# Performance work log

Hardware: AMD Instinct MI355X
Metric: run time of the kernel (lower is better)

Reference implementation:

```python
import jax, jax.numpy as jnp
import numpy as np

N_HEAD = 12
HEAD_DIM = 64
N_EMBD = 768
ATTN_MULT = 0.125
B, T = 2, 2048
NEG_INF = -1e30


def setup_inputs() -> dict:
    key = jax.random.key(0)
    ks = jax.random.split(key, 3)
    x = jax.random.normal(ks[0], (B, T, N_EMBD), dtype=jnp.float32)
    W_attn = jax.random.normal(ks[1], (N_EMBD, 3 * N_HEAD * HEAD_DIM), dtype=jnp.float32) * 0.02
    b_attn = jnp.zeros((3 * N_HEAD * HEAD_DIM,), dtype=jnp.float32)
    W_proj = jax.random.normal(ks[2], (N_HEAD * HEAD_DIM, N_EMBD), dtype=jnp.float32) * 0.02
    b_proj = jnp.zeros((N_EMBD,), dtype=jnp.float32)
    return {"x": x, "W_attn": W_attn, "b_attn": b_attn, "W_proj": W_proj, "b_proj": b_proj}


def reference(x, W_attn, b_attn, W_proj, b_proj):
    Bsz, Tlen, C = x.shape
    H, D = N_HEAD, HEAD_DIM
    qkv = x @ W_attn + b_attn                       # [B,T,3*H*D]
    q, k, v = jnp.split(qkv, 3, axis=-1)
    q = q.reshape(Bsz, Tlen, H, D).transpose(0, 2, 1, 3)   # [B,H,T,D]
    k = k.reshape(Bsz, Tlen, H, D).transpose(0, 2, 1, 3)
    v = v.reshape(Bsz, Tlen, H, D).transpose(0, 2, 1, 3)

    att = jnp.einsum('bhtd,bhsd->bhts', q, k) * ATTN_MULT  # [B,H,T,T]
    causal = jnp.tril(jnp.ones((Tlen, Tlen), dtype=bool))  # [T,T]
    att = jnp.where(causal, att, NEG_INF)

    # selection mask from head 0 (SelectionHeadLinearComboKind.NONE)
    S = jax.nn.relu(att[:, 0:1, :, :])                     # [B,1,T,T]; relu kills -inf
    # protect_bos_token: zero column 0 (key index 0)
    col = jnp.arange(Tlen)
    S = S * (col[None, None, None, :] != 0)
    # prevent_from_masking_myself: zero diagonal
    S = S * (1.0 - jnp.eye(Tlen, dtype=S.dtype))

    # accumulate selection over query (row) axis: ProtectionKind.NONE
    FF = jnp.cumsum(S, axis=-2)                            # [B,1,T,T]
    att = att - FF                                         # broadcast over heads

    p = jax.nn.softmax(att, axis=-1)                       # [B,H,T,T]
    y = jnp.einsum('bhts,bhsd->bhtd', p, v)                # [B,H,T,D]
    y = y.transpose(0, 2, 1, 3).reshape(Bsz, Tlen, H * D)  # [B,T,H*D]
    return y @ W_proj + b_proj
```

## Files before the change

kernel.cpp:

```cpp
#include <hip/hip_runtime.h>
#include <math.h>

#define T 2048
#define NH 12
#define HD 64
#define C3 2304
#define CE 768
#define NB 2

typedef __attribute__((ext_vector_type(8))) short bf16x8;
typedef __attribute__((ext_vector_type(4))) float f32x4;
typedef __attribute__((ext_vector_type(16))) float f32x16;
typedef __attribute__((ext_vector_type(4))) unsigned u32x4;

__device__ inline void bf16split(float a, unsigned short& h, unsigned short& l) {
    unsigned int u = __float_as_uint(a);
    unsigned int r = (u + 0x7FFFu + ((u >> 16) & 1u)) >> 16;
    h = (unsigned short)r;
    float hf = __uint_as_float(r << 16);
    float lo = a - hf;
    unsigned int v = __float_as_uint(lo);
    l = (unsigned short)((v + 0x7FFFu + ((v >> 16) & 1u)) >> 16);
}

// ... 7 lines not shown
__global__ __launch_bounds__(256) void cvt_split_kernel(const float* __restrict__ A,
        unsigned short* __restrict__ H, unsigned short* __restrict__ L) {
    int i = blockIdx.x * 256 + threadIdx.x;
    float4 a0 = *(reinterpret_cast<const float4*>(A) + (size_t)i * 2);
    float4 a1 = *(reinterpret_cast<const float4*>(A) + (size_t)i * 2 + 1);
    float f[8] = {a0.x, a0.y, a0.z, a0.w, a1.x, a1.y, a1.z, a1.w};
    unsigned short h[8], l[8];
    #pragma unroll
    for (int j = 0; j < 8; ++j) bf16split(f[j], h[j], l[j]);
    uint4 hv, lv;
    hv.x = (unsigned)h[0] | ((unsigned)h[1] << 16); hv.y = (unsigned)h[2] | ((unsigned)h[3] << 16);
    hv.z = (unsigned)h[4] | ((unsigned)h[5] << 16); hv.w = (unsigned)h[6] | ((unsigned)h[7] << 16);
    lv.x = (unsigned)l[0] | ((unsigned)l[1] << 16); lv.y = (unsigned)l[2] | ((unsigned)l[3] << 16);
    lv.z = (unsigned)l[4] | ((unsigned)l[5] << 16); lv.w = (unsigned)l[6] | ((unsigned)l[7] << 16);
    reinterpret_cast<uint4*>(H)[i] = hv;
    reinterpret_cast<uint4*>(L)[i] = lv;
}

__global__ __launch_bounds__(256) void cvt_split_T_kernel(const float* __restrict__ W,
        unsigned short* __restrict__ H, unsigned short* __restrict__ L, int K, int N) {
    __shared__ float tile[64][65];
    const int n0 = blockIdx.x * 64, k0 = blockIdx.y * 64;
    const int t = threadIdx.x;
    {
        int r = t >> 2, c4 = (t & 3) * 16;
        #pragma unroll
        for (int u = 0; u < 4; ++u) {
            float4 w = *reinterpret_cast<const float4*>(&W[(size_t)(k0 + r) * N + n0 + c4 + u * 4]);
            tile[r][c4 + u * 4 + 0] = w.x; tile[r][c4 + u * 4 + 1] = w.y;
            tile[r][c4 + u * 4 + 2] = w.z; tile[r][c4 + u * 4 + 3] = w.w;
        }
    }
    __syncthreads();
    {
        int n = t >> 2, kc = (t & 3) * 16;
        unsigned short h[16], l[16];
        #pragma unroll
        for (int j = 0; j < 16; ++j) bf16split(tile[kc + j][n], h[j], l[j]);
        uint4 hv0, hv1, lv0, lv1;
        hv0.x = (unsigned)h[0] | ((unsigned)h[1] << 16);  hv0.y = (unsigned)h[2] | ((unsigned)h[3] << 16);
        hv0.z = (unsigned)h[4] | ((unsigned)h[5] << 16);  hv0.w = (unsigned)h[6] | ((unsigned)h[7] << 16);
        hv1.x = (unsigned)h[8] | ((unsigned)h[9] << 16);  hv1.y = (unsigned)h[10] | ((unsigned)h[11] << 16);
        hv1.z = (unsigned)h[12] | ((unsigned)h[13] << 16); hv1.w = (unsigned)h[14] | ((unsigned)h[15] << 16);
        lv0.x = (unsigned)l[0] | ((unsigned)l[1] << 16);  lv0.y = (unsigned)l[2] | ((unsigned)l[3] << 16);
        lv0.z = (unsigned)l[4] | ((unsigned)l[5] << 16);  lv0.w = (unsigned)l[6] | ((unsigned)l[7] << 16);
        lv1.x = (unsigned)l[8] | ((unsigned)l[9] << 16);  lv1.y = (unsigned)l[10] | ((unsigned)l[11] << 16);
        lv1.z = (unsigned)l[12] | ((unsigned)l[13] << 16); lv1.w = (unsigned)l[14] | ((unsigned)l[15] << 16);
        size_t o = (size_t)(n0 + n) * K + k0 + kc;
        reinterpret_cast<uint4*>(&H[o])[0] = hv0; reinterpret_cast<uint4*>(&H[o])[1] = hv1;
        reinterpret_cast<uint4*>(&L[o])[0] = lv0; reinterpret_cast<uint4*>(&L[o])[1] = lv1;
    }
}

__global__ __launch_bounds__(256) void cvt_qk_kernel(const float* __restrict__ qkv,
        unsigned short* __restrict__ Qh, unsigned short* __restrict__ Ql,
        unsigned short* __restrict__ Kh, unsigned short* __restrict__ Kl) {
    int t = blockIdx.x * 256 + threadIdx.x;
    int dg = t & 7;
    int s = (t >> 3) & (T - 1);
    int bh = t >> 14;
    int b = bh / NH, h = bh % NH;
    const float* qs = qkv + (size_t)(b * T + s) * C3 + h * 64 + dg * 8;
    const float* ks = qs + 768;
    size_t o = ((size_t)bh * T + s) * 64 + dg * 8;
    #pragma unroll
    for (int which = 0; which < 2; ++which) {
        const float* src = (which == 0) ? qs : ks;
        float4 a0 = *reinterpret_cast<const float4*>(src);
        float4 a1 = *reinterpret_cast<const float4*>(src + 4);
        float f[8] = {a0.x, a0.y, a0.z, a0.w, a1.x, a1.y, a1.z, a1.w};
        unsigned short hh[8], ll[8];
        #pragma unroll
        for (int j = 0; j < 8; ++j) bf16split(f[j], hh[j], ll[j]);
        uint4 hv, lv;
        hv.x = (unsigned)hh[0] | ((unsigned)hh[1] << 16); hv.y = (unsigned)hh[2] | ((unsigned)hh[3] << 16);
        hv.z = (unsigned)hh[4] | ((unsigned)hh[5] << 16); hv.w = (unsigned)hh[6] | ((unsigned)hh[7] << 16);
        lv.x = (unsigned)ll[0] | ((unsigned)ll[1] << 16); lv.y = (unsigned)ll[2] | ((unsigned)ll[3] << 16);
        lv.z = (unsigned)ll[4] | ((unsigned)ll[5] << 16); lv.w = (unsigned)ll[6] | ((unsigned)ll[7] << 16);
        if (which == 0) {
            *reinterpret_cast<uint4*>(&Qh[o]) = hv;
            *reinterpret_cast<uint4*>(&Ql[o]) = lv;
        } else {
            *reinterpret_cast<uint4*>(&Kh[o]) = hv;
            *reinterpret_cast<uint4*>(&Kl[o]) = lv;
        }
    }
}

__global__ __launch_bounds__(256) void cvt_kv_vt_kernel(const float* __restrict__ qkv,
        unsigned short* __restrict__ Vh, unsigned short* __restrict__ Vl) {
    __shared__ float tile[64][65];
    const int s0 = blockIdx.x * 64;
    const int bh = blockIdx.y;
    const int b = bh / NH, h = bh % NH;
    const int tid = threadIdx.x;
    {
        int r = tid >> 2, c0 = (tid & 3) * 16;
        const float* src = qkv + (size_t)(b * T + s0 + r) * C3 + 1536 + h * 64 + c0;
        #pragma unroll
        for (int u = 0; u < 4; ++u) {
            float4 w = *reinterpret_cast<const float4*>(src + u * 4);
            tile[r][c0 + u * 4 + 0] = w.x; tile[r][c0 + u * 4 + 1] = w.y;
            tile[r][c0 + u * 4 + 2] = w.z; tile[r][c0 + u * 4 + 3] = w.w;
        }
    }
    __syncthreads();
    {
        int d = tid >> 2, cs = (tid & 3) * 16;
        unsigned short hh[16], ll[16];
        #pragma unroll
        for (int j = 0; j < 16; ++j) bf16split(tile[cs + j][d], hh[j], ll[j]);
        uint4 hv0, hv1, lv0, lv1;
        hv0.x = (unsigned)hh[0] | ((unsigned)hh[1] << 16);  hv0.y = (unsigned)hh[2] | ((unsigned)hh[3] << 16);
        hv0.z = (unsigned)hh[4] | ((unsigned)hh[5] << 16);  hv0.w = (unsigned)hh[6] | ((unsigned)hh[7] << 16);
        hv1.x = (unsigned)hh[8] | ((unsigned)hh[9] << 16);  hv1.y = (unsigned)hh[10] | ((unsigned)hh[11] << 16);
        hv1.z = (unsigned)hh[12] | ((unsigned)hh[13] << 16); hv1.w = (unsigned)hh[14] | ((unsigned)hh[15] << 16);
        lv0.x = (unsigned)ll[0] | ((unsigned)ll[1] << 16);  lv0.y = (unsigned)ll[2] | ((unsigned)ll[3] << 16);
        lv0.z = (unsigned)ll[4] | ((unsigned)ll[5] << 16);  lv0.w = (unsigned)ll[6] | ((unsigned)ll[7] << 16);
        lv1.x = (unsigned)ll[8] | ((unsigned)ll[9] << 16);  lv1.y = (unsigned)ll[10] | ((unsigned)ll[11] << 16);
        lv1.z = (unsigned)ll[12] | ((unsigned)ll[13] << 16); lv1.w = (unsigned)ll[14] | ((unsigned)ll[15] << 16);
        size_t o = ((size_t)bh * 64 + d) * T + s0 + cs;
        reinterpret_cast<uint4*>(&Vh[o])[0] = hv0; reinterpret_cast<uint4*>(&Vh[o])[1] = hv1;
        reinterpret_cast<uint4*>(&Vl[o])[0] = lv0; reinterpret_cast<uint4*>(&Vl[o])[1] = lv1;
    }
}

#define LDST 40
__global__ __launch_bounds__(256) void gemm_mfma_kernel(
        const unsigned short* __restrict__ Ah, const unsigned short* __restrict__ Al,
        const unsigned short* __restrict__ Bh, const unsigned short* __restrict__ Bl,
        const float* __restrict__ bias, float* __restrict__ Cm,
        int M, int N, int K) {
    __shared__ unsigned short lA[2][128 * LDST];
    __shared__ unsigned short lB[2][128 * LDST];
    const int tid = threadIdx.x;
    const int bm = blockIdx.y * 128, bn = blockIdx.x * 128;
    const int lane = tid & 63, wid = tid >> 6;
    const int wr = wid >> 1, wc = wid & 1;
    f32x4 acc[4][4];
    #pragma unroll
    for (int i = 0; i < 4; ++i)
        #pragma unroll
        for (int j = 0; j < 4; ++j) acc[i][j] = (f32x4){0.f, 0.f, 0.f, 0.f};
    const int srow = tid >> 2, sk8 = (tid & 3) * 8;
    const int arb = wr * 64 + (lane & 15);
    const int brb = wc * 64 + (lane & 15);
    const int koff = (lane >> 4) * 8;
    for (int k0 = 0; k0 < K; k0 += 32) {
        __syncthreads();
        #pragma unroll
        for (int c = 0; c < 2; ++c) {
            int row = srow + 64 * c;
            uint4 va = *reinterpret_cast<const uint4*>(&Ah[(size_t)(bm + row) * K + k0 + sk8]);
            uint4 vb = *reinterpret_cast<const uint4*>(&Al[(size_t)(bm + row) * K + k0 + sk8]);
            uint4 vc = *reinterpret_cast<const uint4*>(&Bh[(size_t)(bn + row) * K + k0 + sk8]);
            uint4 vd = *reinterpret_cast<const uint4*>(&Bl[(size_t)(bn + row) * K + k0 + sk8]);
            *reinterpret_cast<uint4*>(&lA[0][row * LDST + sk8]) = va;
            *reinterpret_cast<uint4*>(&lA[1][row * LDST + sk8]) = vb;
            *reinterpret_cast<uint4*>(&lB[0][row * LDST + sk8]) = vc;
            *reinterpret_cast<uint4*>(&lB[1][row * LDST + sk8]) = vd;
        }
        __syncthreads();
        bf16x8 fa[2][4], fb[2][4];
        #pragma unroll
        for (int fi = 0; fi < 4; ++fi) {
            fa[0][fi] = *reinterpret_cast<const bf16x8*>(&lA[0][(arb + fi * 16) * LDST + koff]);
            fa[1][fi] = *reinterpret_cast<const bf16x8*>(&lA[1][(arb + fi * 16) * LDST + koff]);
            fb[0][fi] = *reinterpret_cast<const bf16x8*>(&lB[0][(brb + fi * 16) * LDST + koff]);
            fb[1][fi] = *reinterpret_cast<const bf16x8*>(&lB[1][(brb + fi * 16) * LDST + koff]);
        }
        #pragma unroll
        for (int fi = 0; fi < 4; ++fi)
            #pragma unroll
            for (int fj = 0; fj < 4; ++fj) {
                acc[fi][fj] = __builtin_amdgcn_mfma_f32_16x16x32_bf16(fa[0][fi], fb[0][fj], acc[fi][fj], 0, 0, 0);
                acc[fi][fj] = __builtin_amdgcn_mfma_f32_16x16x32_bf16(fa[0][fi], fb[1][fj], acc[fi][fj], 0, 0, 0);
                acc[fi][fj] = __builtin_amdgcn_mfma_f32_16x16x32_bf16(fa[1][fi], fb[0][fj], acc[fi][fj], 0, 0, 0);
            }
    }
    #pragma unroll
    for (int fj = 0; fj < 4; ++fj) {
        int col = bn + wc * 64 + fj * 16 + (lane & 15);
        float bv = bias[col];
        #pragma unroll
        for (int fi = 0; fi < 4; ++fi) {
            int row0 = bm + wr * 64 + fi * 16 + (lane >> 4) * 4;
            #pragma unroll
            for (int p = 0; p < 4; ++p)
                Cm[(size_t)(row0 + p) * N + col] = acc[fi][fj][p] + bv;
        }
    }
}

__global__ __launch_bounds__(256) void gemm_bias_kernel(
        const float* __restrict__ A, const float* __restrict__ B,
        const float* __restrict__ bias, float* __restrict__ Cm,
        int M, int N, int K) {
    __shared__ float As[16][64];
    __shared__ float Bs[16][68];
    const int tid = threadIdx.x;
    const int ty = tid >> 4, tx = tid & 15;
    const int bm = blockIdx.y * 64, bn = blockIdx.x * 64;
    float acc[4][4] = {};
    for (int k0 = 0; k0 < K; k0 += 16) {
        {
            int r = tid >> 2;
            int kk = (tid & 3) * 4;
            float4 a = *reinterpret_cast<const float4*>(&A[(size_t)(bm + r) * K + k0 + kk]);
            As[kk + 0][r] = a.x; As[kk + 1][r] = a.y; As[kk + 2][r] = a.z; As[kk + 3][r] = a.w;
        }
        {
            int kk = tid >> 4;
            int c = (tid & 15) * 4;
            *reinterpret_cast<float4*>(&Bs[kk][c]) =
                *reinterpret_cast<const float4*>(&B[(size_t)(k0 + kk) * N + bn + c]);
        }
        __syncthreads();
        #pragma unroll
        for (int kk = 0; kk < 16; ++kk) {
            float4 a4 = *reinterpret_cast<const float4*>(&As[kk][ty * 4]);
            float4 b4 = *reinterpret_cast<const float4*>(&Bs[kk][tx * 4]);
            float av[4] = {a4.x, a4.y, a4.z, a4.w};
            float bv[4] = {b4.x, b4.y, b4.z, b4.w};
            #pragma unroll
            for (int i = 0; i < 4; ++i)
                #pragma unroll
                for (int j = 0; j < 4; ++j)
                    acc[i][j] = fmaf(av[i], bv[j], acc[i][j]);
        }
        __syncthreads();
    }
    #pragma unroll
    for (int i = 0; i < 4; ++i) {
        int row = bm + ty * 4 + i;
        #pragma unroll
        for (int j = 0; j < 4; ++j) {
            int col = bn + tx * 4 + j;
            Cm[(size_t)row * N + col] = acc[i][j] + bias[col];
        }
    }
}

#define FST 72

__global__ __launch_bounds__(256) void s0_mfma_kernel(
        const unsigned short* __restrict__ Qh, const unsigned short* __restrict__ Ql,
        const unsigned short* __restrict__ Kh, const unsigned short* __restrict__ Kl,
        float* __restrict__ S) {
    const int kb = blockIdx.x * 64, qb = blockIdx.y * 64, b = blockIdx.z;
    const int tid = threadIdx.x;
    float* Sb = S + (size_t)b * T * T;
    if (kb > qb) {
        const int ty = tid >> 4, tx = tid & 15;
        #pragma unroll
        for (int i = 0; i < 4; ++i) {
            float4 z = {0.f, 0.f, 0.f, 0.f};
            *reinterpret_cast<float4*>(&Sb[(size_t)(qb + ty * 4 + i) * T + kb + tx * 4]) = z;
        }
        return;
    }
    const int lane = tid & 63, w = tid >> 6;
    const int fr = lane & 15, fg = lane >> 4;
    __shared__ unsigned short Ks[2][64 * FST];
    const int hb0 = b * NH;
    {
        const int sr = tid >> 2, sc0 = (tid & 3) * 16;
        const unsigned short* kh = Kh + ((size_t)hb0 * T + kb + sr) * 64 + sc0;
        const unsigned short* kl = Kl + ((size_t)hb0 * T + kb + sr) * 64 + sc0;
        uint4 a0 = reinterpret_cast<const uint4*>(kh)[0];
        uint4 a1 = reinterpret_cast<const uint4*>(kh)[1];
        uint4 b0 = reinterpret_cast<const uint4*>(kl)[0];
        uint4 b1 = reinterpret_cast<const uint4*>(kl)[1];
        *reinterpret_cast<uint4*>(&Ks[0][sr * FST + sc0 + 0]) = a0;
        *reinterpret_cast<uint4*>(&Ks[0][sr * FST + sc0 + 8]) = a1;
        *reinterpret_cast<uint4*>(&Ks[1][sr * FST + sc0 + 0]) = b0;
        *reinterpret_cast<uint4*>(&Ks[1][sr * FST + sc0 + 8]) = b1;
    }
    bf16x8 qh[2], ql[2];
    #pragma unroll
    for (int ks = 0; ks < 2; ++ks) {
        size_t qo = ((size_t)hb0 * T + qb + w * 16 + fr) * 64 + ks * 32 + fg * 8;
        qh[ks] = *reinterpret_cast<const bf16x8*>(&Qh[qo]);
        ql[ks] = *reinterpret_cast<const bf16x8*>(&Ql[qo]);
    }
    __syncthreads();
    f32x4 qk[4];
    #pragma unroll
    for (int fj = 0; fj < 4; ++fj) qk[fj] = (f32x4){0.f, 0.f, 0.f, 0.f};
    #pragma unroll
    for (int ks = 0; ks < 2; ++ks) {
        bf16x8 kbh[4], kbl[4];
        #pragma unroll
        for (int fj = 0; fj < 4; ++fj) {
            kbh[fj] = *reinterpret_cast<const bf16x8*>(&Ks[0][(fj * 16 + fr) * FST + ks * 32 + fg * 8]);
            kbl[fj] = *reinterpret_cast<const bf16x8*>(&Ks[1][(fj * 16 + fr) * FST + ks * 32 + fg * 8]);
        }
        #pragma unroll
        for (int fj = 0; fj < 4; ++fj) {
            qk[fj] = __builtin_amdgcn_mfma_f32_16x16x32_bf16(qh[ks], kbh[fj], qk[fj], 0, 0, 0);
            qk[fj] = __builtin_amdgcn_mfma_f32_16x16x32_bf16(qh[ks], kbl[fj], qk[fj], 0, 0, 0);
            qk[fj] = __builtin_amdgcn_mfma_f32_16x16x32_bf16(ql[ks], kbh[fj], qk[fj], 0, 0, 0);
        }
    }
    #pragma unroll
    for (int p = 0; p < 4; ++p) {
        int t = qb + w * 16 + fg * 4 + p;
        #pragma unroll
        for (int fj = 0; fj < 4; ++fj) {
            int s = kb + fj * 16 + fr;
            float v = qk[fj][p] * 0.125f;
            Sb[(size_t)t * T + s] = (s >= 1 && s < t) ? fmaxf(v, 0.0f) : 0.0f;
        }
    }
}

__global__ __launch_bounds__(256) void s0_kernel(const float* __restrict__ qkv,
                                                 float* __restrict__ S) {
    const int kb = blockIdx.x * 64, qb = blockIdx.y * 64, b = blockIdx.z;
    const int tid = threadIdx.x, ty = tid >> 4, tx = tid & 15;
    float* Sb = S + (size_t)b * T * T;
    if (kb > qb) {
        #pragma unroll
        for (int i = 0; i < 4; ++i) {
            int row = qb + ty * 4 + i;
            float4 z = {0.f, 0.f, 0.f, 0.f};
            *reinterpret_cast<float4*>(&Sb[(size_t)row * T + kb + tx * 4]) = z;
        }
        return;
    }
    __shared__ float Qt[64][68];
    __shared__ float Kt[64][68];
    {
        int r = tid >> 2;
        int c0 = (tid & 3) * 16;
        const float* qrow = qkv + (size_t)(b * T + qb + r) * C3 + 0;
        const float* krow = qkv + (size_t)(b * T + kb + r) * C3 + 768;
        #pragma unroll
        for (int u = 0; u < 4; ++u) {
            float4 q4 = *reinterpret_cast<const float4*>(&qrow[c0 + u * 4]);
            float4 k4 = *reinterpret_cast<const float4*>(&krow[c0 + u * 4]);
            int d = c0 + u * 4;
            Qt[d + 0][r] = q4.x; Qt[d + 1][r] = q4.y; Qt[d + 2][r] = q4.z; Qt[d + 3][r] = q4.w;
            Kt[d + 0][r] = k4.x; Kt[d + 1][r] = k4.y; Kt[d + 2][r] = k4.z; Kt[d + 3][r] = k4.w;
        }
    }
    __syncthreads();
    float acc[4][4] = {};
    #pragma unroll
    for (int d = 0; d < 64; ++d) {
        float4 qv = *reinterpret_cast<const float4*>(&Qt[d][ty * 4]);
        float4 kv = *reinterpret_cast<const float4*>(&Kt[d][tx * 4]);
        float qa[4] = {qv.x, qv.y, qv.z, qv.w};
        float ka[4] = {kv.x, kv.y, kv.z, kv.w};
        #pragma unroll
        for (int i = 0; i < 4; ++i)
            #pragma unroll
            for (int j = 0; j < 4; ++j)
                acc[i][j] = fmaf(qa[i], ka[j], acc[i][j]);
    }
    #pragma unroll
    for (int i = 0; i < 4; ++i) {
        int t = qb + ty * 4 + i;
        float o[4];
        #pragma unroll
        for (int j = 0; j < 4; ++j) {
            int s = kb + tx * 4 + j;
            float v = acc[i][j] * 0.125f;
            o[j] = (s >= 1 && s < t) ? fmaxf(v, 0.0f) : 0.0f;
        }
        float4 o4 = {o[0], o[1], o[2], o[3]};
        *reinterpret_cast<float4*>(&Sb[(size_t)t * T + kb + tx * 4]) = o4;
    }
}

__global__ __launch_bounds__(256) void colsum_kernel(const float* __restrict__ S,
                                                     float* __restrict__ Psum) {
    int s = blockIdx.x * 256 + threadIdx.x;
    int j = blockIdx.y, b = blockIdx.z;
    const float* Sb = S + (size_t)b * T * T;
    float sum = 0.f;
    for (int r = 0; r < 64; ++r) sum += Sb[(size_t)(j * 64 + r) * T + s];
    Psum[((size_t)b * 32 + j) * T + s] = sum;
}

__global__ __launch_bounds__(256) void scanseg_kernel(float* __restrict__ Psum) {
    int s = blockIdx.x * 256 + threadIdx.x;
    int b = blockIdx.y;
    float run = 0.f;
    for (int j = 0; j < 32; ++j) {
        size_t idx = ((size_t)b * 32 + j) * T + s;
        float v = Psum[idx];
        Psum[idx] = run;
        run += v;
    }
}

__global__ __launch_bounds__(256) void ffscan_kernel(float* __restrict__ S,
                                                     const float* __restrict__ Psum) {
    int s = blockIdx.x * 256 + threadIdx.x;
    int j = blockIdx.y, b = blockIdx.z;
    float run = Psum[((size_t)b * 32 + j) * T + s];
    float* Sb = S + (size_t)b * T * T;
    for (int r = 0; r < 64; ++r) {
        size_t idx = (size_t)(j * 64 + r) * T + s;
        run += Sb[idx];
        Sb[idx] = run;
    }
}

__device__ const int FTQ[40] = {15,15,15,15,14,14,14,13,13,13,12,12,12,11,11,11,10,10,9,9,8,8,7,7,6,5,4,3,14,10,6,2,13,9,5,1,12,8,4,0};
__device__ const int FK0[40] = {0,8,16,24,0,8,16,0,8,16,0,8,16,0,8,16,0,8,0,8,0,8,0,8,0,0,0,0,24,16,8,0,24,16,8,0,24,16,8,0};
__device__ const int FK1[40] = {8,16,24,32,8,16,24,8,16,24,8,16,24,8,16,24,8,16,8,16,8,16,8,16,8,8,8,8,30,22,14,6,28,20,12,4,26,18,10,2};
__device__ const int FCB[12] = {0,2,4,6,8,11,14,17,20,24,28,32};

__global__ __launch_bounds__(256) void flash_mfma_kernel(
        const unsigned short* __restrict__ Qh, const unsigned short* __restrict__ Ql,
        const unsigned short* __restrict__ Kh, const unsigned short* __restrict__ Kl,
        const unsigned short* __restrict__ Vth, const unsigned short* __restrict__ Vtl,
        const float* __restrict__ FF, float* __restrict__ Y,
        float* __restrict__ PART) {
    const int hb = blockIdx.x;
    const int h = hb % NH, b = hb / NH;
    const int u = blockIdx.y;
    const int tq = FTQ[u], kt0 = FK0[u], kt1 = FK1[u];
    const int qb = tq * 128;
    const int tid = threadIdx.x;
    const int lane = tid & 63, w = tid >> 6;
    const int q31 = lane & 31, hi = lane >> 5;
    const int trow = qb + w * 32 + q31;
    __shared__ unsigned short KS[2][64 * FST];
    __shared__ unsigned short VS[2][64 * FST];

    bf16x8 qfh[4], qfl[4];
    #pragma unroll
    for (int dblk = 0; dblk < 4; ++dblk) {
        size_t qo = ((size_t)hb * T + trow) * 64 + dblk * 16 + hi * 8;
        qfh[dblk] = *reinterpret_cast<const bf16x8*>(&Qh[qo]);
        qfl[dblk] = *reinterpret_cast<const bf16x8*>(&Ql[qo]);
    }

    f32x16 oacc0 = (f32x16)(0.f), oacc1 = (f32x16)(0.f);
    float m = -1e30f, l = 0.f;
    const float* FFb = FF + (size_t)b * T * T;
    const int sr = tid >> 2, sc0 = (tid & 3) * 16;

    for (int kt = kt0; kt < kt1; ++kt) {
        const int kb = kt * 64;
        __syncthreads();
        {
            const unsigned short* ksrc = Kh + ((size_t)hb * T + kb + sr) * 64 + sc0;
            const unsigned short* ksrl = Kl + ((size_t)hb * T + kb + sr) * 64 + sc0;
            const unsigned short* vsrc = Vth + ((size_t)hb * 64 + sr) * T + kb + sc0;
            const unsigned short* vsrl = Vtl + ((size_t)hb * 64 + sr) * T + kb + sc0;
            uint4 k0v = reinterpret_cast<const uint4*>(ksrc)[0];
            uint4 k1v = reinterpret_cast<const uint4*>(ksrc)[1];
            uint4 k2v = reinterpret_cast<const uint4*>(ksrl)[0];
            uint4 k3v = reinterpret_cast<const uint4*>(ksrl)[1];
            uint4 v0v = reinterpret_cast<const uint4*>(vsrc)[0];
            uint4 v1v = reinterpret_cast<const uint4*>(vsrc)[1];
            uint4 v2v = reinterpret_cast<const uint4*>(vsrl)[0];
            uint4 v3v = reinterpret_cast<const uint4*>(vsrl)[1];
            *reinterpret_cast<uint4*>(&KS[0][sr * FST + sc0 + 0]) = k0v;
            *reinterpret_cast<uint4*>(&KS[0][sr * FST + sc0 + 8]) = k1v;
            *reinterpret_cast<uint4*>(&KS[1][sr * FST + sc0 + 0]) = k2v;
            *reinterpret_cast<uint4*>(&KS[1][sr * FST + sc0 + 8]) = k3v;
            *reinterpret_cast<uint4*>(&VS[0][sr * FST + sc0 + 0]) = v0v;
            *reinterpret_cast<uint4*>(&VS[0][sr * FST + sc0 + 8]) = v1v;
            *reinterpret_cast<uint4*>(&VS[1][sr * FST + sc0 + 0]) = v2v;
            *reinterpret_cast<uint4*>(&VS[1][sr * FST + sc0 + 8]) = v3v;
        }
        __syncthreads();
        f32x16 acc[2];
// ... 46 lines not shown
        l = l * scale + rs;
        m = mn;
        oacc0 *= scale; oacc1 *= scale;
        unsigned wh[2][4][2], wl[2][4][2];
        #pragma unroll
        for (int sb = 0; sb < 2; ++sb)
            #pragma unroll
            for (int bq = 0; bq < 4; ++bq)
                #pragma unroll
                for (int h2 = 0; h2 < 2; ++h2)
                    packP(pv[sb][4 * bq + 2 * h2], pv[sb][4 * bq + 2 * h2 + 1],
                          wh[sb][bq][h2], wl[sb][bq][h2]);
        #pragma unroll
        for (int kk = 0; kk < 4; ++kk) {
            const int sb = kk >> 1;
            const int b0 = 2 * (kk & 1), b1 = b0 + 1;
            unsigned sh_b1_0 = (unsigned)__shfl_xor((int)wh[sb][b1][0], 32);
            unsigned sh_b1_1 = (unsigned)__shfl_xor((int)wh[sb][b1][1], 32);
            unsigned sh_b0_0 = (unsigned)__shfl_xor((int)wh[sb][b0][0], 32);
            unsigned sh_b0_1 = (unsigned)__shfl_xor((int)wh[sb][b0][1], 32);
            unsigned sl_b1_0 = (unsigned)__shfl_xor((int)wl[sb][b1][0], 32);
            unsigned sl_b1_1 = (unsigned)__shfl_xor((int)wl[sb][b1][1], 32);
            unsigned sl_b0_0 = (unsigned)__shfl_xor((int)wl[sb][b0][0], 32);
            unsigned sl_b0_1 = (unsigned)__shfl_xor((int)wl[sb][b0][1], 32);
            u32x4 th, tl;
            th[0] = hi ? sh_b1_0 : wh[sb][b0][0];
            th[1] = hi ? sh_b1_1 : wh[sb][b0][1];
            th[2] = hi ? wh[sb][b1][0] : sh_b0_0;
            th[3] = hi ? wh[sb][b1][1] : sh_b0_1;
            tl[0] = hi ? sl_b1_0 : wl[sb][b0][0];
            tl[1] = hi ? sl_b1_1 : wl[sb][b0][1];
            tl[2] = hi ? wl[sb][b1][0] : sl_b0_0;
            tl[3] = hi ? wl[sb][b1][1] : sl_b0_1;
            bf16x8 pbh = __builtin_bit_cast(bf16x8, th);
            bf16x8 pbl = __builtin_bit_cast(bf16x8, tl);
            {
                bf16x8 vfh = *reinterpret_cast<const bf16x8*>(&VS[0][(q31) * FST + kk * 16 + hi * 8]);
                bf16x8 vfl = *reinterpret_cast<const bf16x8*>(&VS[1][(q31) * FST + kk * 16 + hi * 8]);
                oacc0 = __builtin_amdgcn_mfma_f32_32x32x16_bf16(vfh, pbh, oacc0, 0, 0, 0);
                oacc0 = __builtin_amdgcn_mfma_f32_32x32x16_bf16(vfh, pbl, oacc0, 0, 0, 0);
                oacc0 = __builtin_amdgcn_mfma_f32_32x32x16_bf16(vfl, pbh, oacc0, 0, 0, 0);
            }
            {
                bf16x8 vfh = *reinterpret_cast<const bf16x8*>(&VS[0][(32 + q31) * FST + kk * 16 + hi * 8]);
                bf16x8 vfl = *reinterpret_cast<const bf16x8*>(&VS[1][(32 + q31) * FST + kk * 16 + hi * 8]);
                oacc1 = __builtin_amdgcn_mfma_f32_32x32x16_bf16(vfh, pbh, oacc1, 0, 0, 0);
                oacc1 = __builtin_amdgcn_mfma_f32_32x32x16_bf16(vfh, pbl, oacc1, 0, 0, 0);
                oacc1 = __builtin_amdgcn_mfma_f32_32x32x16_bf16(vfl, pbh, oacc1, 0, 0, 0);
            }
        }
    }
    if (tq < 4) {
        float inv = 1.f / l;
        float* Yrow = Y + (size_t)(b * T + trow) * CE + h * 64;
        #pragma unroll
        for (int g = 0; g < 4; ++g) {
            float4 o0 = {oacc0[4 * g + 0] * inv, oacc0[4 * g + 1] * inv,
                         oacc0[4 * g + 2] * inv, oacc0[4 * g + 3] * inv};
            float4 o1 = {oacc1[4 * g + 0] * inv, oacc1[4 * g + 1] * inv,
                         oacc1[4 * g + 2] * inv, oacc1[4 * g + 3] * inv};
            *reinterpret_cast<float4*>(&Yrow[g * 8 + hi * 4]) = o0;
            *reinterpret_cast<float4*>(&Yrow[32 + g * 8 + hi * 4]) = o1;
        }
    } else {
        const int ci = FCB[tq - 4] + (kt0 >> 3);
        float* Ob = PART + (size_t)(hb * 36 + ci) * 8448;
        const int rr = w * 32 + q31;
        #pragma unroll
        for (int g = 0; g < 4; ++g) {
            float4 o0 = {oacc0[4 * g + 0], oacc0[4 * g + 1], oacc0[4 * g + 2], oacc0[4 * g + 3]};
            float4 o1 = {oacc1[4 * g + 0], oacc1[4 * g + 1], oacc1[4 * g + 2], oacc1[4 * g + 3]};
            *reinterpret_cast<float4*>(&Ob[rr * 64 + g * 8 + hi * 4]) = o0;
            *reinterpret_cast<float4*>(&Ob[rr * 64 + 32 + g * 8 + hi * 4]) = o1;
        }
        if (hi == 0) { Ob[8192 + rr] = m; Ob[8192 + 128 + rr] = l; }
    }
}

__global__ __launch_bounds__(256) void merge128_kernel(const float* __restrict__ PART,
                                                       float* __restrict__ Y) {
    const int hb = blockIdx.x;
    const int tq = 4 + blockIdx.y;
    const int h = hb % NH, b = hb / NH;
    const int nch = (tq >= 12) ? 4 : (tq >= 8) ? 3 : 2;
    const float* base = PART + (size_t)(hb * 36 + FCB[tq - 4]) * 8448;
    const int tid = threadIdx.x;
    const int r = tid >> 1, half = tid & 1;
    float mm[4], la[4];
    float M = -1e30f;
    #pragma unroll
    for (int c = 0; c < 4; ++c) {
        int cc = (c < nch) ? c : 0;
        float mv = base[(size_t)cc * 8448 + 8192 + r];
        float lv = base[(size_t)cc * 8448 + 8192 + 128 + r];
        mm[c] = (c < nch) ? mv : -1e30f;
        la[c] = (c < nch) ? lv : 0.f;
        M = fmaxf(M, mm[c]);
    }
    float a[4], L = 0.f;
    #pragma unroll
    for (int c = 0; c < 4; ++c) {
        a[c] = (c < nch) ? __expf(mm[c] - M) : 0.f;
        L += a[c] * la[c];
    }
    float inv = 1.f / L;
    const int t = tq * 128 + r;
    float* Yrow = Y + (size_t)(b * T + t) * CE + h * 64 + half * 32;
    #pragma unroll
    for (int uu = 0; uu < 8; ++uu) {
        float ax = 0.f, ay = 0.f, az = 0.f, aw = 0.f;
        #pragma unroll
        for (int c = 0; c < 4; ++c) {
            int cc = (c < nch) ? c : 0;
            float4 x = *reinterpret_cast<const float4*>(
                &base[(size_t)cc * 8448 + r * 64 + half * 32 + uu * 4]);
            ax += a[c] * x.x; ay += a[c] * x.y; az += a[c] * x.z; aw += a[c] * x.w;
        }
        float4 y = {ax * inv, ay * inv, az * inv, aw * inv};
        *reinterpret_cast<float4*>(&Yrow[uu * 4]) = y;
    }
}

__global__ __launch_bounds__(256) void flash_kernel(const float* __restrict__ qkv,
                                                    const float* __restrict__ FF,
                                                    float* __restrict__ Y,
                                                    float* __restrict__ PO,
                                                    float* __restrict__ PML,
                                                    int split) {
    const int hb = blockIdx.x;
    const int h = hb % NH, b = hb / NH;
    int qt, kt0, kt1, mode;
    if (split) {
        const int u = blockIdx.y;
        if (u < 16)      { qt = 16 + u; kt0 = 0;  kt1 = 16;     mode = 1; }
        else if (u < 32) { qt = 31 - u; kt0 = 0;  kt1 = qt + 1; mode = 0; }
        else             { qt = 63 - u; kt0 = 16; kt1 = qt + 1; mode = 2; }
    } else {
        qt = 31 - blockIdx.y; kt0 = 0; kt1 = qt + 1; mode = 0;
    }
    const int qb = qt * 64;
    const int tid = threadIdx.x, ty = tid >> 4, tx = tid & 15;
    __shared__ float Qt[64][68];
    __shared__ float KtPs[64][68];
    __shared__ float Vs[64][68];
    const int r = tid >> 2, c0 = (tid & 3) * 16;
    {
        const float* qrow = qkv + (size_t)(b * T + qb + r) * C3 + h * 64;
        #pragma unroll
        for (int u = 0; u < 4; ++u) {
            float4 q4 = *reinterpret_cast<const float4*>(&qrow[c0 + u * 4]);
            int d = c0 + u * 4;
            Qt[d + 0][r] = q4.x; Qt[d + 1][r] = q4.y; Qt[d + 2][r] = q4.z; Qt[d + 3][r] = q4.w;
        }
    }
    float m[4], l[4], O[4][4];
    #pragma unroll
    for (int i = 0; i < 4; ++i) {
        m[i] = -1e30f; l[i] = 0.f;
        #pragma unroll
        for (int j = 0; j < 4; ++j) O[i][j] = 0.f;
    }
    const float* FFb = FF + (size_t)b * T * T;
    for (int kt = kt0; kt < kt1; ++kt) {
        const int kb = kt * 64;
        __syncthreads();
        {
            const float* krow = qkv + (size_t)(b * T + kb + r) * C3 + 768 + h * 64;
            const float* vrow = qkv + (size_t)(b * T + kb + r) * C3 + 1536 + h * 64;
            #pragma unroll
            for (int u = 0; u < 4; ++u) {
                float4 k4 = *reinterpret_cast<const float4*>(&krow[c0 + u * 4]);
                int d = c0 + u * 4;
// ... 112 lines not shown
    const float* O1  = PO  + (size_t)(NB * NH * 16) * 4096 + (size_t)p * 4096;
    const float* ml0 = PML + (size_t)p * 128;
    const float* ml1 = PML + (size_t)(NB * NH * 16) * 128  + (size_t)p * 128;
    const int tid = threadIdx.x;
    const int r = tid >> 2, c0 = (tid & 3) * 16;
    float m0 = ml0[r], l0 = ml0[64 + r];
    float m1 = ml1[r], l1 = ml1[64 + r];
    float M  = fmaxf(m0, m1);
    float a0 = __expf(m0 - M), a1 = __expf(m1 - M);
    float inv = 1.f / (a0 * l0 + a1 * l1);
    const int t = qt * 64 + r;
    float* Yrow = Y + (size_t)(b * T + t) * CE + h * 64;
    #pragma unroll
    for (int u = 0; u < 4; ++u) {
        float4 x0 = *reinterpret_cast<const float4*>(&O0[r * 64 + c0 + u * 4]);
        float4 x1 = *reinterpret_cast<const float4*>(&O1[r * 64 + c0 + u * 4]);
        float4 y;
        y.x = (a0 * x0.x + a1 * x1.x) * inv;
        y.y = (a0 * x0.y + a1 * x1.y) * inv;
        y.z = (a0 * x0.z + a1 * x1.z) * inv;
        y.w = (a0 * x0.w + a1 * x1.w) * inv;
        *reinterpret_cast<float4*>(&Yrow[c0 + u * 4]) = y;
    }
}

extern "C" void kernel_launch(void* const* d_in, const int* in_sizes, int n_in,
                              void* d_out, int out_size, void* d_ws, size_t ws_size,
                              hipStream_t stream) {
    const float* x      = (const float*)d_in[0];
    const float* W_attn = (const float*)d_in[1];
    const float* b_attn = (const float*)d_in[2];
    const float* W_proj = (const float*)d_in[3];
    const float* b_proj = (const float*)d_in[4];
    float* out = (float*)d_out;

    char* ws = (char*)d_ws;
    const size_t QKV_BYTES = (size_t)NB * T * C3 * 4;
    const size_t S_BYTES   = (size_t)NB * T * T * 4;
    const size_t P_BYTES   = (size_t)NB * 32 * T * 4;
    const size_t Y_BYTES   = (size_t)NB * T * CE * 4;
    const size_t PO_BYTES  = (size_t)2 * NB * NH * 16 * 4096 * 4;
    const size_t PML_BYTES = (size_t)2 * NB * NH * 16 * 128 * 4;
    const size_t PLANE_X   = (size_t)NB * T * CE * 2;
    const size_t PLANE_WA  = (size_t)C3 * CE * 2;
    const size_t PLANE_WP  = (size_t)CE * CE * 2;
    const size_t PLANE_KV  = (size_t)NB * NH * T * 64 * 2;

    const size_t U_OFF  = QKV_BYTES + S_BYTES + P_BYTES + Y_BYTES;
    const size_t U_SIZE = PO_BYTES + PML_BYTES;
    const size_t W_OFF  = U_OFF + U_SIZE;
    const size_t KV_OFF = W_OFF + 2 * PLANE_WA + 2 * PLANE_WP;

    float* qkv  = (float*)ws;
    float* S    = (float*)(ws + QKV_BYTES);
    float* Psum = (float*)(ws + QKV_BYTES + S_BYTES);
    float* Yb   = (float*)(ws + QKV_BYTES + S_BYTES + P_BYTES);
    float* PO   = (float*)(ws + U_OFF);
    float* PML  = (float*)(ws + U_OFF + PO_BYTES);
    unsigned short* Xh  = (unsigned short*)(ws + U_OFF);
    unsigned short* Xl  = (unsigned short*)(ws + U_OFF + PLANE_X);
    unsigned short* Qhp = Xh;
    unsigned short* Qlp = Xl;
    unsigned short* Yh  = Xh;
    unsigned short* Yl  = Xl;
    unsigned short* WAh = (unsigned short*)(ws + W_OFF);
    unsigned short* WAl = (unsigned short*)(ws + W_OFF + PLANE_WA);
    unsigned short* WPh = (unsigned short*)(ws + W_OFF + 2 * PLANE_WA);
    unsigned short* WPl = (unsigned short*)(ws + W_OFF + 2 * PLANE_WA + PLANE_WP);
    unsigned short* Khp = (unsigned short*)(ws + KV_OFF);
    unsigned short* Klp = (unsigned short*)(ws + KV_OFF + PLANE_KV);
    unsigned short* VTh = (unsigned short*)(ws + KV_OFF + 2 * PLANE_KV);
    unsigned short* VTl = (unsigned short*)(ws + KV_OFF + 3 * PLANE_KV);
    float* PART = qkv;

    const size_t NEED_SPLIT = U_OFF + U_SIZE;
    const size_t NEED_MFMA  = KV_OFF;
    const size_t NEED_KV    = KV_OFF + 4 * PLANE_KV;
    const int split = (ws_size >= NEED_SPLIT) ? 1 : 0;
    const int mfma  = (ws_size >= NEED_MFMA) ? 1 : 0;
    const int kv    = (ws_size >= NEED_KV && mfma) ? 1 : 0;

    const int M = NB * T;

    if (mfma) {
        cvt_split_T_kernel<<<dim3(C3 / 64, CE / 64), 256, 0, stream>>>(W_attn, WAh, WAl, CE, C3);
        cvt_split_T_kernel<<<dim3(CE / 64, CE / 64), 256, 0, stream>>>(W_proj, WPh, WPl, CE, CE);
        cvt_split_kernel<<<dim3((M * CE / 8) / 256), 256, 0, stream>>>(x, Xh, Xl);
        gemm_mfma_kernel<<<dim3(C3 / 128, M / 128), 256, 0, stream>>>(Xh, Xl, WAh, WAl, b_attn, qkv, M, C3, CE);
    } else {
        gemm_bias_kernel<<<dim3(C3 / 64, M / 64), 256, 0, stream>>>(x, W_attn, b_attn, qkv, M, C3, CE);
    }
    if (kv) {
        cvt_qk_kernel<<<dim3((NB * NH * T * 8) / 256), 256, 0, stream>>>(qkv, Qhp, Qlp, Khp, Klp);
        cvt_kv_vt_kernel<<<dim3(T / 64, NB * NH), 256, 0, stream>>>(qkv, VTh, VTl);
        s0_mfma_kernel<<<dim3(T / 64, T / 64, NB), 256, 0, stream>>>(Qhp, Qlp, Khp, Klp, S);
    } else {
        s0_kernel<<<dim3(T / 64, T / 64, NB), 256, 0, stream>>>(qkv, S);
    }
    colsum_kernel<<<dim3(T / 256, 32, NB), 256, 0, stream>>>(S, Psum);
    scanseg_kernel<<<dim3(T / 256, NB), 256, 0, stream>>>(Psum);
    ffscan_kernel<<<dim3(T / 256, 32, NB), 256, 0, stream>>>(S, Psum);
    if (kv) {
        flash_mfma_kernel<<<dim3(NB * NH, 40), 256, 0, stream>>>(Qhp, Qlp, Khp, Klp, VTh, VTl, S, Yb, PART);
        merge128_kernel<<<dim3(NB * NH, 12), 256, 0, stream>>>(PART, Yb);
    } else if (split) {
        flash_kernel<<<dim3(NB * NH, 48), 256, 0, stream>>>(qkv, S, Yb, PO, PML, 1);
        merge_kernel<<<dim3(NB * NH * 16), 256, 0, stream>>>(PO, PML, Yb);
    } else {
        flash_kernel<<<dim3(NB * NH, 32), 256, 0, stream>>>(qkv, S, Yb, PO, PML, 0);
    }
    if (mfma) {
        cvt_split_kernel<<<dim3((M * CE / 8) / 256), 256, 0, stream>>>(Yb, Yh, Yl);
        gemm_mfma_kernel<<<dim3(CE / 128, M / 128), 256, 0, stream>>>(Yh, Yl, WPh, WPl, b_proj, out, M, CE, CE);
    } else {
        gemm_bias_kernel<<<dim3(CE / 64, M / 64), 256, 0, stream>>>(Yb, W_proj, b_proj, out, M, CE, CE);
    }
}
```

Measured before the change: 260.5 us.

## Fuse bf16 splitting into QKV GEMM, attention epilogue, and S0 column sums

The QKV GEMM now writes Q and K directly as hi/lo bf16 planes in head-major layout, plus a compact V buffer. This removes the full fp32 qkv round trip and the separate cvt_qk kernel. s0_mfma now produces the per-block column partial sums, which removes colsum_kernel, and scanseg loads all 32 values before writing. The flash and merge epilogues emit the split bf16 Y directly, so the cvt_split pass before the output projection is no longer needed. The tradeoffs are scattered 2-byte stores in the GEMM epilogue and extra conversion work inside the attention kernels.

```diff
diff --git a/kernel.cpp b/kernel.cpp
--- a/kernel.cpp
+++ b/kernel.cpp
@@ -83,51 +83,15 @@
     }
 }
 
-__global__ __launch_bounds__(256) void cvt_qk_kernel(const float* __restrict__ qkv,
-        unsigned short* __restrict__ Qh, unsigned short* __restrict__ Ql,
-        unsigned short* __restrict__ Kh, unsigned short* __restrict__ Kl) {
-    int t = blockIdx.x * 256 + threadIdx.x;
-    int dg = t & 7;
-    int s = (t >> 3) & (T - 1);
-    int bh = t >> 14;
-    int b = bh / NH, h = bh % NH;
-    const float* qs = qkv + (size_t)(b * T + s) * C3 + h * 64 + dg * 8;
-    const float* ks = qs + 768;
-    size_t o = ((size_t)bh * T + s) * 64 + dg * 8;
-    #pragma unroll
-    for (int which = 0; which < 2; ++which) {
-        const float* src = (which == 0) ? qs : ks;
-        float4 a0 = *reinterpret_cast<const float4*>(src);
-        float4 a1 = *reinterpret_cast<const float4*>(src + 4);
-        float f[8] = {a0.x, a0.y, a0.z, a0.w, a1.x, a1.y, a1.z, a1.w};
-        unsigned short hh[8], ll[8];
-        #pragma unroll
-        for (int j = 0; j < 8; ++j) bf16split(f[j], hh[j], ll[j]);
-        uint4 hv, lv;
-        hv.x = (unsigned)hh[0] | ((unsigned)hh[1] << 16); hv.y = (unsigned)hh[2] | ((unsigned)hh[3] << 16);
-        hv.z = (unsigned)hh[4] | ((unsigned)hh[5] << 16); hv.w = (unsigned)hh[6] | ((unsigned)hh[7] << 16);
-        lv.x = (unsigned)ll[0] | ((unsigned)ll[1] << 16); lv.y = (unsigned)ll[2] | ((unsigned)ll[3] << 16);
-        lv.z = (unsigned)ll[4] | ((unsigned)ll[5] << 16); lv.w = (unsigned)ll[6] | ((unsigned)ll[7] << 16);
-        if (which == 0) {
-            *reinterpret_cast<uint4*>(&Qh[o]) = hv;
-            *reinterpret_cast<uint4*>(&Ql[o]) = lv;
-        } else {
-            *reinterpret_cast<uint4*>(&Kh[o]) = hv;
-            *reinterpret_cast<uint4*>(&Kl[o]) = lv;
-        }
-    }
-}
-
-__global__ __launch_bounds__(256) void cvt_kv_vt_kernel(const float* __restrict__ qkv,
+__global__ __launch_bounds__(256) void cvt_kv_vt_kernel(const float* __restrict__ Vtmp,
         unsigned short* __restrict__ Vh, unsigned short* __restrict__ Vl) {
     __shared__ float tile[64][65];
     const int s0 = blockIdx.x * 64;
     const int bh = blockIdx.y;
-    const int b = bh / NH, h = bh % NH;
     const int tid = threadIdx.x;
     {
         int r = tid >> 2, c0 = (tid & 3) * 16;
-        const float* src = qkv + (size_t)(b * T + s0 + r) * C3 + 1536 + h * 64 + c0;
+        const float* src = Vtmp + ((size_t)bh * T + s0 + r) * 64 + c0;
         #pragma unroll
         for (int u = 0; u < 4; ++u) {
             float4 w = *reinterpret_cast<const float4*>(src + u * 4);
@@ -219,6 +183,92 @@
             #pragma unroll
             for (int p = 0; p < 4; ++p)
                 Cm[(size_t)(row0 + p) * N + col] = acc[fi][fj][p] + bv;
+        }
+    }
+}
+
+__global__ __launch_bounds__(256) void gemm_qkv_mfma_kernel(
+        const unsigned short* __restrict__ Ah, const unsigned short* __restrict__ Al,
+        const unsigned short* __restrict__ Bh, const unsigned short* __restrict__ Bl,
+        const float* __restrict__ bias,
+        unsigned short* __restrict__ Qh, unsigned short* __restrict__ Ql,
+        unsigned short* __restrict__ Kh, unsigned short* __restrict__ Kl,
+        float* __restrict__ Vtmp) {
+    const int N = C3, K = CE;
+    __shared__ unsigned short lA[2][128 * LDST];
+    __shared__ unsigned short lB[2][128 * LDST];
+    const int tid = threadIdx.x;
+    const int bm = blockIdx.y * 128, bn = blockIdx.x * 128;
+    const int lane = tid & 63, wid = tid >> 6;
+    const int wr = wid >> 1, wc = wid & 1;
+    f32x4 acc[4][4];
+    #pragma unroll
+    for (int i = 0; i < 4; ++i)
+        #pragma unroll
+        for (int j = 0; j < 4; ++j) acc[i][j] = (f32x4){0.f, 0.f, 0.f, 0.f};
+    const int srow = tid >> 2, sk8 = (tid & 3) * 8;
+    const int arb = wr * 64 + (lane & 15);
+    const int brb = wc * 64 + (lane & 15);
+    const int koff = (lane >> 4) * 8;
+    for (int k0 = 0; k0 < K; k0 += 32) {
+        __syncthreads();
+        #pragma unroll
+        for (int c = 0; c < 2; ++c) {
+            int row = srow + 64 * c;
+            uint4 va = *reinterpret_cast<const uint4*>(&Ah[(size_t)(bm + row) * K + k0 + sk8]);
+            uint4 vb = *reinterpret_cast<const uint4*>(&Al[(size_t)(bm + row) * K + k0 + sk8]);
+            uint4 vc = *reinterpret_cast<const uint4*>(&Bh[(size_t)(bn + row) * K + k0 + sk8]);
+            uint4 vd = *reinterpret_cast<const uint4*>(&Bl[(size_t)(bn + row) * K + k0 + sk8]);
+            *reinterpret_cast<uint4*>(&lA[0][row * LDST + sk8]) = va;
+            *reinterpret_cast<uint4*>(&lA[1][row * LDST + sk8]) = vb;
+            *reinterpret_cast<uint4*>(&lB[0][row * LDST + sk8]) = vc;
+            *reinterpret_cast<uint4*>(&lB[1][row * LDST + sk8]) = vd;
+        }
+        __syncthreads();
+        bf16x8 fa[2][4], fb[2][4];
+        #pragma unroll
+        for (int fi = 0; fi < 4; ++fi) {
+            fa[0][fi] = *reinterpret_cast<const bf16x8*>(&lA[0][(arb + fi * 16) * LDST + koff]);
+            fa[1][fi] = *reinterpret_cast<const bf16x8*>(&lA[1][(arb + fi * 16) * LDST + koff]);
+            fb[0][fi] = *reinterpret_cast<const bf16x8*>(&lB[0][(brb + fi * 16) * LDST + koff]);
+            fb[1][fi] = *reinterpret_cast<const bf16x8*>(&lB[1][(brb + fi * 16) * LDST + koff]);
+        }
+        #pragma unroll
+        for (int fi = 0; fi < 4; ++fi)
+            #pragma unroll
+            for (int fj = 0; fj < 4; ++fj) {
+                acc[fi][fj] = __builtin_amdgcn_mfma_f32_16x16x32_bf16(fa[0][fi], fb[0][fj], acc[fi][fj], 0, 0, 0);
+                acc[fi][fj] = __builtin_amdgcn_mfma_f32_16x16x32_bf16(fa[0][fi], fb[1][fj], acc[fi][fj], 0, 0, 0);
+                acc[fi][fj] = __builtin_amdgcn_mfma_f32_16x16x32_bf16(fa[1][fi], fb[0][fj], acc[fi][fj], 0, 0, 0);
+            }
+    }
+    const int colbase = bn + wc * 64;
+    const int region = colbase / 768;
+    const int h = (colbase % 768) >> 6;
+    #pragma unroll
+    for (int fj = 0; fj < 4; ++fj) {
+        int col = colbase + fj * 16 + (lane & 15);
+        float bv = bias[col];
+        int d = fj * 16 + (lane & 15);
+        #pragma unroll
+        for (int fi = 0; fi < 4; ++fi) {
+            int row0 = bm + wr * 64 + fi * 16 + (lane >> 4) * 4;
+            #pragma unroll
+            for (int p = 0; p < 4; ++p) {
+                int tg = row0 + p;
+                int bb = tg >> 11, t = tg & (T - 1);
+                size_t o = ((size_t)(bb * NH + h) * T + t) * 64 + d;
+                float val = acc[fi][fj][p] + bv;
+                if (region == 0) {
+                    unsigned short hh, ll; bf16split(val, hh, ll);
+                    Qh[o] = hh; Ql[o] = ll;
+                } else if (region == 1) {
+                    unsigned short hh, ll; bf16split(val, hh, ll);
+                    Kh[o] = hh; Kl[o] = ll;
+                } else {
+                    Vtmp[o] = val;
+                }
+            }
         }
     }
 }
@@ -277,7 +327,7 @@
 __global__ __launch_bounds__(256) void s0_mfma_kernel(
         const unsigned short* __restrict__ Qh, const unsigned short* __restrict__ Ql,
         const unsigned short* __restrict__ Kh, const unsigned short* __restrict__ Kl,
-        float* __restrict__ S) {
+        float* __restrict__ S, float* __restrict__ Psum) {
     const int kb = blockIdx.x * 64, qb = blockIdx.y * 64, b = blockIdx.z;
     const int tid = threadIdx.x;
     float* Sb = S + (size_t)b * T * T;
@@ -288,11 +338,13 @@
             float4 z = {0.f, 0.f, 0.f, 0.f};
             *reinterpret_cast<float4*>(&Sb[(size_t)(qb + ty * 4 + i) * T + kb + tx * 4]) = z;
         }
+        if (tid < 64) Psum[((size_t)(b * 32 + (qb >> 6)) * T) + kb + tid] = 0.f;
         return;
     }
     const int lane = tid & 63, w = tid >> 6;
     const int fr = lane & 15, fg = lane >> 4;
     __shared__ unsigned short Ks[2][64 * FST];
+    __shared__ float csum[4][64];
     const int hb0 = b * NH;
     {
         const int sr = tid >> 2, sc0 = (tid & 3) * 16;
@@ -333,6 +385,7 @@
             qk[fj] = __builtin_amdgcn_mfma_f32_16x16x32_bf16(ql[ks], kbh[fj], qk[fj], 0, 0, 0);
         }
     }
+    float colsum[4] = {0.f, 0.f, 0.f, 0.f};
     #pragma unroll
     for (int p = 0; p < 4; ++p) {
         int t = qb + w * 16 + fg * 4 + p;
@@ -340,8 +393,24 @@
         for (int fj = 0; fj < 4; ++fj) {
             int s = kb + fj * 16 + fr;
             float v = qk[fj][p] * 0.125f;
-            Sb[(size_t)t * T + s] = (s >= 1 && s < t) ? fmaxf(v, 0.0f) : 0.0f;
-        }
+            float o = (s >= 1 && s < t) ? fmaxf(v, 0.0f) : 0.0f;
+            Sb[(size_t)t * T + s] = o;
+            colsum[fj] += o;
+        }
+    }
+    #pragma unroll
+    for (int fj = 0; fj < 4; ++fj) {
+        colsum[fj] += __shfl_xor(colsum[fj], 16);
+        colsum[fj] += __shfl_xor(colsum[fj], 32);
+    }
+    if (lane < 16) {
+        #pragma unroll
+        for (int fj = 0; fj < 4; ++fj) csum[w][fj * 16 + lane] = colsum[fj];
+    }
+    __syncthreads();
+    if (tid < 64) {
+        float v = csum[0][tid] + csum[1][tid] + csum[2][tid] + csum[3][tid];
+        Psum[((size_t)(b * 32 + (qb >> 6)) * T) + kb + tid] = v;
     }
 }
 
@@ -417,12 +486,15 @@
 __global__ __launch_bounds__(256) void scanseg_kernel(float* __restrict__ Psum) {
     int s = blockIdx.x * 256 + threadIdx.x;
     int b = blockIdx.y;
+    float v[32];
+    #pragma unroll
+    for (int j = 0; j < 32; ++j)
+        v[j] = Psum[((size_t)(b * 32 + j)) * T + s];
     float run = 0.f;
+    #pragma unroll
     for (int j = 0; j < 32; ++j) {
-        size_t idx = ((size_t)b * 32 + j) * T + s;
-        float v = Psum[idx];
-        Psum[idx] = run;
-        run += v;
+        Psum[((size_t)(b * 32 + j)) * T + s] = run;
+        run += v[j];
     }
 }
 
@@ -448,7 +520,8 @@
         const unsigned short* __restrict__ Qh, const unsigned short* __restrict__ Ql,
         const unsigned short* __restrict__ Kh, const unsigned short* __restrict__ Kl,
         const unsigned short* __restrict__ Vth, const unsigned short* __restrict__ Vtl,
-        const float* __restrict__ FF, float* __restrict__ Y,
+        const float* __restrict__ FF,
+        unsigned short* __restrict__ Yh, unsigned short* __restrict__ Yl,
         float* __restrict__ PART) {
     const int hb = blockIdx.x;
     const int h = hb % NH, b = hb / NH;
@@ -601,15 +674,23 @@
     }
     if (tq < 4) {
         float inv = 1.f / l;
-        float* Yrow = Y + (size_t)(b * T + trow) * CE + h * 64;
+        size_t ybase = ((size_t)(b * T + trow)) * CE + h * 64;
         #pragma unroll
         for (int g = 0; g < 4; ++g) {
-            float4 o0 = {oacc0[4 * g + 0] * inv, oacc0[4 * g + 1] * inv,
-                         oacc0[4 * g + 2] * inv, oacc0[4 * g + 3] * inv};
-            float4 o1 = {oacc1[4 * g + 0] * inv, oacc1[4 * g + 1] * inv,
-                         oacc1[4 * g + 2] * inv, oacc1[4 * g + 3] * inv};
-            *reinterpret_cast<float4*>(&Yrow[g * 8 + hi * 4]) = o0;
-            *reinterpret_cast<float4*>(&Yrow[32 + g * 8 + hi * 4]) = o1;
+            unsigned short h0[4], l0[4], h1[4], l1[4];
+            #pragma unroll
+            for (int i = 0; i < 4; ++i) {
+                bf16split(oacc0[4 * g + i] * inv, h0[i], l0[i]);
+                bf16split(oacc1[4 * g + i] * inv, h1[i], l1[i]);
+            }
+            uint2 ph0 = {(unsigned)h0[0] | ((unsigned)h0[1] << 16), (unsigned)h0[2] | ((unsigned)h0[3] << 16)};
+            uint2 pl0 = {(unsigned)l0[0] | ((unsigned)l0[1] << 16), (unsigned)l0[2] | ((unsigned)l0[3] << 16)};
+            uint2 ph1 = {(unsigned)h1[0] | ((unsigned)h1[1] << 16), (unsigned)h1[2] | ((unsigned)h1[3] << 16)};
+            uint2 pl1 = {(unsigned)l1[0] | ((unsigned)l1[1] << 16), (unsigned)l1[2] | ((unsigned)l1[3] << 16)};
+            *reinterpret_cast<uint2*>(&Yh[ybase + g * 8 + hi * 4]) = ph0;
+            *reinterpret_cast<uint2*>(&Yl[ybase + g * 8 + hi * 4]) = pl0;
+            *reinterpret_cast<uint2*>(&Yh[ybase + 32 + g * 8 + hi * 4]) = ph1;
+            *reinterpret_cast<uint2*>(&Yl[ybase + 32 + g * 8 + hi * 4]) = pl1;
         }
     } else {
         const int ci = FCB[tq - 4] + (kt0 >> 3);
@@ -627,7 +708,8 @@
 }
 
 __global__ __launch_bounds__(256) void merge128_kernel(const float* __restrict__ PART,
-                                                       float* __restrict__ Y) {
+                                                       unsigned short* __restrict__ Yh,
+                                                       unsigned short* __restrict__ Yl) {
     const int hb = blockIdx.x;
     const int tq = 4 + blockIdx.y;
     const int h = hb % NH, b = hb / NH;
@@ -654,7 +736,7 @@
     }
     float inv = 1.f / L;
     const int t = tq * 128 + r;
-    float* Yrow = Y + (size_t)(b * T + t) * CE + h * 64 + half * 32;
+    size_t ybase = ((size_t)(b * T + t)) * CE + h * 64 + half * 32;
     #pragma unroll
     for (int uu = 0; uu < 8; ++uu) {
         float ax = 0.f, ay = 0.f, az = 0.f, aw = 0.f;
@@ -665,8 +747,13 @@
                 &base[(size_t)cc * 8448 + r * 64 + half * 32 + uu * 4]);
             ax += a[c] * x.x; ay += a[c] * x.y; az += a[c] * x.z; aw += a[c] * x.w;
         }
-        float4 y = {ax * inv, ay * inv, az * inv, aw * inv};
-        *reinterpret_cast<float4*>(&Yrow[uu * 4]) = y;
+        unsigned short hh[4], ll[4];
+        bf16split(ax * inv, hh[0], ll[0]); bf16split(ay * inv, hh[1], ll[1]);
+        bf16split(az * inv, hh[2], ll[2]); bf16split(aw * inv, hh[3], ll[3]);
+        uint2 ph = {(unsigned)hh[0] | ((unsigned)hh[1] << 16), (unsigned)hh[2] | ((unsigned)hh[3] << 16)};
+        uint2 pl = {(unsigned)ll[0] | ((unsigned)ll[1] << 16), (unsigned)ll[2] | ((unsigned)ll[3] << 16)};
+        *reinterpret_cast<uint2*>(&Yh[ybase + uu * 4]) = ph;
+        *reinterpret_cast<uint2*>(&Yl[ybase + uu * 4]) = pl;
     }
 }
 
@@ -885,17 +972,19 @@
     const size_t KV_OFF = W_OFF + 2 * PLANE_WA + 2 * PLANE_WP;
 
     float* qkv  = (float*)ws;
+    float* Vtmp = (float*)ws;
+    float* PART = (float*)ws;
     float* S    = (float*)(ws + QKV_BYTES);
     float* Psum = (float*)(ws + QKV_BYTES + S_BYTES);
     float* Yb   = (float*)(ws + QKV_BYTES + S_BYTES + P_BYTES);
+    unsigned short* Qhp = (unsigned short*)(ws + QKV_BYTES + S_BYTES + P_BYTES);
+    unsigned short* Qlp = (unsigned short*)(ws + QKV_BYTES + S_BYTES + P_BYTES + PLANE_X);
     float* PO   = (float*)(ws + U_OFF);
     float* PML  = (float*)(ws + U_OFF + PO_BYTES);
     unsigned short* Xh  = (unsigned short*)(ws + U_OFF);
     unsigned short* Xl  = (unsigned short*)(ws + U_OFF + PLANE_X);
-    unsigned short* Qhp = Xh;
-    unsigned short* Qlp = Xl;
-    unsigned short* Yh  = Xh;
-    unsigned short* Yl  = Xl;
+    unsigned short* Yhp = Xh;
+    unsigned short* Ylp = Xl;
     unsigned short* WAh = (unsigned short*)(ws + W_OFF);
     unsigned short* WAl = (unsigned short*)(ws + W_OFF + PLANE_WA);
     unsigned short* WPh = (unsigned short*)(ws + W_OFF + 2 * PLANE_WA);
@@ -904,7 +993,6 @@
     unsigned short* Klp = (unsigned short*)(ws + KV_OFF + PLANE_KV);
     unsigned short* VTh = (unsigned short*)(ws + KV_OFF + 2 * PLANE_KV);
     unsigned short* VTl = (unsigned short*)(ws + KV_OFF + 3 * PLANE_KV);
-    float* PART = qkv;
 
     const size_t NEED_SPLIT = U_OFF + U_SIZE;
     const size_t NEED_MFMA  = KV_OFF;
@@ -914,6 +1002,24 @@
     const int kv    = (ws_size >= NEED_KV && mfma) ? 1 : 0;
 
     const int M = NB * T;
+
+    if (kv) {
+        cvt_split_T_kernel<<<dim3(C3 / 64, CE / 64), 256, 0, stream>>>(W_attn, WAh, WAl, CE, C3);
+        cvt_split_T_kernel<<<dim3(CE / 64, CE / 64), 256, 0, stream>>>(W_proj, WPh, WPl, CE, CE);
+        cvt_split_kernel<<<dim3((M * CE / 8) / 256), 256, 0, stream>>>(x, Xh, Xl);
+        gemm_qkv_mfma_kernel<<<dim3(C3 / 128, M / 128), 256, 0, stream>>>(
+            Xh, Xl, WAh, WAl, b_attn, Qhp, Qlp, Khp, Klp, Vtmp);
+        cvt_kv_vt_kernel<<<dim3(T / 64, NB * NH), 256, 0, stream>>>(Vtmp, VTh, VTl);
+        s0_mfma_kernel<<<dim3(T / 64, T / 64, NB), 256, 0, stream>>>(Qhp, Qlp, Khp, Klp, S, Psum);
+        scanseg_kernel<<<dim3(T / 256, NB), 256, 0, stream>>>(Psum);
+        ffscan_kernel<<<dim3(T / 256, 32, NB), 256, 0, stream>>>(S, Psum);
+        flash_mfma_kernel<<<dim3(NB * NH, 40), 256, 0, stream>>>(
+            Qhp, Qlp, Khp, Klp, VTh, VTl, S, Yhp, Ylp, PART);
+        merge128_kernel<<<dim3(NB * NH, 12), 256, 0, stream>>>(PART, Yhp, Ylp);
+        gemm_mfma_kernel<<<dim3(CE / 128, M / 128), 256, 0, stream>>>(
+            Yhp, Ylp, WPh, WPl, b_proj, out, M, CE, CE);
+        return;
+    }
 
     if (mfma) {
         cvt_split_T_kernel<<<dim3(C3 / 64, CE / 64), 256, 0, stream>>>(W_attn, WAh, WAl, CE, C3);
@@ -923,28 +1029,19 @@
     } else {
         gemm_bias_kernel<<<dim3(C3 / 64, M / 64), 256, 0, stream>>>(x, W_attn, b_attn, qkv, M, C3, CE);
     }
-    if (kv) {
-        cvt_qk_kernel<<<dim3((NB * NH * T * 8) / 256), 256, 0, stream>>>(qkv, Qhp, Qlp, Khp, Klp);
-        cvt_kv_vt_kernel<<<dim3(T / 64, NB * NH), 256, 0, stream>>>(qkv, VTh, VTl);
-        s0_mfma_kernel<<<dim3(T / 64, T / 64, NB), 256, 0, stream>>>(Qhp, Qlp, Khp, Klp, S);
-    } else {
-        s0_kernel<<<dim3(T / 64, T / 64, NB), 256, 0, stream>>>(qkv, S);
-    }
+    s0_kernel<<<dim3(T / 64, T / 64, NB), 256, 0, stream>>>(qkv, S);
     colsum_kernel<<<dim3(T / 256, 32, NB), 256, 0, stream>>>(S, Psum);
     scanseg_kernel<<<dim3(T / 256, NB), 256, 0, stream>>>(Psum);
     ffscan_kernel<<<dim3(T / 256, 32, NB), 256, 0, stream>>>(S, Psum);
-    if (kv) {
-        flash_mfma_kernel<<<dim3(NB * NH, 40), 256, 0, stream>>>(Qhp, Qlp, Khp, Klp, VTh, VTl, S, Yb, PART);
-        merge128_kernel<<<dim3(NB * NH, 12), 256, 0, stream>>>(PART, Yb);
-    } else if (split) {
+    if (split) {
         flash_kernel<<<dim3(NB * NH, 48), 256, 0, stream>>>(qkv, S, Yb, PO, PML, 1);
         merge_kernel<<<dim3(NB * NH * 16), 256, 0, stream>>>(PO, PML, Yb);
     } else {
         flash_kernel<<<dim3(NB * NH, 32), 256, 0, stream>>>(qkv, S, Yb, PO, PML, 0);
     }
     if (mfma) {
-        cvt_split_kernel<<<dim3((M * CE / 8) / 256), 256, 0, stream>>>(Yb, Yh, Yl);
-        gemm_mfma_kernel<<<dim3(CE / 128, M / 128), 256, 0, stream>>>(Yh, Yl, WPh, WPl, b_proj, out, M, CE, CE);
+        cvt_split_kernel<<<dim3((M * CE / 8) / 256), 256, 0, stream>>>(Yb, Xh, Xl);
+        gemm_mfma_kernel<<<dim3(CE / 128, M / 128), 256, 0, stream>>>(Xh, Xl, WPh, WPl, b_proj, out, M, CE, CE);
     } else {
         gemm_bias_kernel<<<dim3(CE / 64, M / 64), 256, 0, stream>>>(Yb, W_proj, b_proj, out, M, CE, CE);
     }
```

Measured after the change: 251.6 us. 3.4% less time.
